# Kernel optimization log

Measured on AMD Instinct MI355X. Metric: run time of the kernel, lower is better.

The kernel has to match this reference:

```python
import jax, jax.numpy as jnp
import numpy as np

E, NB, B, N = 2, 2, 8, 512          # experts, blocks per stack, batch, nodes
SEQ_LEN, CIN, CONV, END = 12, 2, 32, 64
NFE1, SS1 = 4, 0.25                  # outer (backward-time) Euler steps / step size
NFE2, SS2 = 2, 0.5                   # graph-diffusion Euler steps / step size
RF = max(SEQ_LEN, NFE1 * 6 + CIN)    # receptive field = 26 (max kernel 7 -> shrink 6/step)


def setup_inputs() -> dict:
    ks = iter(jax.random.split(jax.random.key(0), 64))

    def nrm(shape, s=0.1):
        return jax.random.normal(next(ks), shape, dtype=jnp.float32) * s

    inp = {
        "X": jax.random.normal(next(ks), (B, SEQ_LEN, N, CIN), dtype=jnp.float32),
        "adj": jax.random.uniform(next(ks), (N, N), dtype=jnp.float32),
        "expert_weights": jnp.ones((E,), jnp.float32),
        "W_start": nrm((E, NB, CONV, CIN)), "b_start": nrm((E, NB, CONV)),
    }
    for t in ("f", "g"):
        for k in (2, 3, 5, 7):
            inp["W_%s%d" % (t, k)] = nrm((E, NB, CONV // 4, CONV, 1, k))
        inp["b_%s" % t] = nrm((E, NB, CONV))
    for t in ("gc1", "gc2"):
        inp["W_" + t] = nrm((E, NB, CONV, (NFE2 + 1) * CONV))
        inp["b_" + t] = nrm((E, NB, CONV))
    for t in ("bc", "fc"):
        inp["W_%s1" % t] = nrm((E, NB, END, CONV)); inp["b_%s1" % t] = nrm((E, NB, END))
        inp["W_%s2" % t] = nrm((E, NB, SEQ_LEN, END)); inp["b_%s2" % t] = nrm((E, NB, SEQ_LEN))
    return inp


def _conv1x1(x, W, b):  # 1x1 Conv2d over NCHW layout
    return jnp.einsum('bchw,oc->bohw', x, W) + b[None, :, None, None]


def _inception(x, Ws, b):  # DilatedInception, dilation=1, kernels (1,2/3/5/7)
    dn = ('NCHW', 'OIHW', 'NCHW')
    ys = [jax.lax.conv_general_dilated(x, W, (1, 1), 'VALID', dimension_numbers=dn) for W in Ws]
    Lm = ys[-1].shape[3]  # crop all branches to the shortest (kernel-7) length
    return jnp.concatenate([y[..., -Lm:] for y in ys], axis=1) + b[None, :, None, None]


def _cgpode(x, A, W, b):  # Euler ODE graph diffusion, concat states, 1x1 mlp
    outs, cur = [x], x
    for _ in range(NFE2):
        cur = cur + SS2 * jnp.einsum('bcwl,vw->bcvl', cur, A)
        outs.append(cur)
    return _conv1x1(jnp.concatenate(outs, axis=1), W, b)


def _forward(X, adj, expert_weights, W_start, b_start,
             W_f2, W_f3, W_f5, W_f7, b_f, W_g2, W_g3, W_g5, W_g7, b_g,
             W_gc1, b_gc1, W_gc2, b_gc2,
             W_bc1, b_bc1, W_bc2, b_bc2, W_fc1, b_fc1, W_fc2, b_fc2):
    n = adj.shape[0]
    A1 = adj + jnp.eye(n, dtype=adj.dtype)     # set_adj: D^-1/2 (A+I) D^-1/2
    di = jnp.sum(A1, axis=1) ** -0.5
    An = di[:, None] * A1 * di[None, :]
    AnT = An.T

    def block(Xb, e, k):  # STBlock; Xb: [B, L, N, C] -> (backcast, forecast)
        x = jnp.transpose(Xb, (0, 3, 2, 1))    # [B, C, N, L]
        x = jnp.pad(x, ((0, 0), (0, 0), (0, 0), (RF - SEQ_LEN, 0)))
        x = _conv1x1(x, W_start[e, k], b_start[e, k])
        Wf = (W_f2[e, k], W_f3[e, k], W_f5[e, k], W_f7[e, k])
        Wg = (W_g2[e, k], W_g3[e, k], W_g5[e, k], W_g7[e, k])
        cur_len = RF
        for _ in range(NFE1):                  # backward-time Euler: x <- x - SS1*enc(x)
            xi = x[..., -cur_len:]             # stateful intermediate_seq_len crop
            h = jnp.tanh(_inception(xi, Wf, b_f[e, k])) * jax.nn.sigmoid(_inception(xi, Wg, b_g[e, k]))
            g = _cgpode(h, An, W_gc1[e, k], b_gc1[e, k]) + _cgpode(h, AnT, W_gc2[e, k], b_gc2[e, k])
            g = jnp.pad(g, ((0, 0), (0, 0), (0, 0), (RF - g.shape[3], 0)))
            x = x - SS1 * g
            cur_len -= 6
        x = x[..., -CIN:]                      # keep last in_dim steps
        mu = jnp.mean(x, axis=(1, 2, 3), keepdims=True)
        var = jnp.mean((x - mu) ** 2, axis=(1, 2, 3), keepdims=True)
        xn = (x - mu) * jax.lax.rsqrt(var + 1e-5)  # layer_norm over shape[1:], no affine
        bc = _conv1x1(jax.nn.relu(_conv1x1(xn, W_bc1[e, k], b_bc1[e, k])), W_bc2[e, k], b_bc2[e, k])
        fc = _conv1x1(jax.nn.relu(_conv1x1(xn, W_fc1[e, k], b_fc1[e, k])), W_fc2[e, k], b_fc2[e, k])[..., -1:]
        return bc, fc

    total = jnp.zeros((X.shape[0], SEQ_LEN, n, 1), X.dtype)
    for e in range(E):                         # independent experts (n_stacks=1 each)
        bkc = X
        fct = jnp.zeros((X.shape[0], SEQ_LEN, n, 1), X.dtype)
        for k in range(NB):                    # residual block stacking inside the stack
            b_, f_ = block(bkc, e, k)
            bkc = bkc - b_
            fct = fct + f_
        total = total + expert_weights[e] * fct
    return total


def reference(X, adj, expert_weights, W_start, b_start, W_f2, W_f3, W_f5, W_f7, b_f, W_g2, W_g3, W_g5, W_g7, b_g, W_gc1, b_gc1, W_gc2, b_gc2, W_bc1, b_bc1, W_bc2, b_bc2, W_fc1, b_fc1, W_fc2, b_fc2):
    return _forward(X, adj, expert_weights, W_start, b_start, W_f2, W_f3, W_f5, W_f7, b_f, W_g2, W_g3, W_g5, W_g7, b_g, W_gc1, b_gc1, W_gc2, b_gc2, W_bc1, b_bc1, W_bc2, b_bc2, W_fc1, b_fc1, W_fc2, b_fc2)
```

## Files before the change

### kernel.cpp

```cpp
#include <hip/hip_runtime.h>
#include <stddef.h>

#define EE 2
#define NBK 2
#define BATCH 8

typedef unsigned short ushort_t;
typedef short bf16x8 __attribute__((ext_vector_type(8)));
typedef float f32x4 __attribute__((ext_vector_type(4)));
typedef unsigned short u16x4 __attribute__((ext_vector_type(4)));

__device__ __forceinline__ ushort_t f2bf(float f) {
    unsigned int u = __float_as_uint(f);
    u += 0x7FFF + ((u >> 16) & 1);
    return (ushort_t)(u >> 16);
}
__device__ __forceinline__ float bf2f(ushort_t h) {
    return __uint_as_float(((unsigned int)h) << 16);
}

__global__ __launch_bounds__(256) void k_rowsum(const float* __restrict__ adj,
                                                float* __restrict__ di) {
    int v = blockIdx.x;
    int tid = threadIdx.x;
    float s = 0.f;
    for (int w = tid; w < 512; w += 256)
        s += adj[v * 512 + w] + (w == v ? 1.f : 0.f);
    for (int off = 32; off; off >>= 1) s += __shfl_down(s, off);
    __shared__ float red[4];
    if ((tid & 63) == 0) red[tid >> 6] = s;
    __syncthreads();
    if (tid == 0) {
        float t = red[0] + red[1] + red[2] + red[3];
        di[v] = rsqrtf(t);
    }
}

__global__ __launch_bounds__(256) void k_norm(const float* __restrict__ adj,
                                              const float* __restrict__ di,
                                              ushort_t* __restrict__ An,
                                              ushort_t* __restrict__ AnT) {
    int idx = blockIdx.x * 256 + threadIdx.x;
    int v = idx >> 9, w = idx & 511;
    float a = adj[idx] + (v == w ? 1.f : 0.f);
    ushort_t val = f2bf(di[v] * a * di[w]);
    An[idx] = val;
    AnT[w * 512 + v] = val;
}

__global__ __launch_bounds__(256) void k_An2(
    const ushort_t* __restrict__ Anb, const ushort_t* __restrict__ AnTb,
    ushort_t* __restrict__ An2, ushort_t* __restrict__ An2T) {
    int tid = threadIdx.x;
    int w = tid >> 6, lane = tid & 63;
    int l15 = lane & 15, lg = lane >> 4;
    int wbase = blockIdx.x * 256 + w * 64;
    int n0 = blockIdx.y * 64;
    f32x4 acc[4][4] = {};
    const ushort_t* Ap = Anb + (size_t)(wbase + l15) * 512 + lg * 8;
    const ushort_t* Bp = AnTb + (size_t)(n0 + l15) * 512 + lg * 8;
    bf16x8 avC[4], bvC[4], avN[4], bvN[4];
#pragma unroll
    for (int i = 0; i < 4; ++i) {
        avC[i] = *(const bf16x8*)(Ap + (size_t)i * 16 * 512);
        bvC[i] = *(const bf16x8*)(Bp + (size_t)i * 16 * 512);
    }
#pragma unroll 2
    for (int k0 = 0; k0 < 512; k0 += 32) {
        int kn = k0 + 32;
        if (kn < 512) {
#pragma unroll
            for (int i = 0; i < 4; ++i) {
                avN[i] = *(const bf16x8*)(Ap + (size_t)i * 16 * 512 + kn);
                bvN[i] = *(const bf16x8*)(Bp + (size_t)i * 16 * 512 + kn);
            }
        }
#pragma unroll
        for (int mf = 0; mf < 4; ++mf)
#pragma unroll
            for (int nf = 0; nf < 4; ++nf)
                acc[mf][nf] = __builtin_amdgcn_mfma_f32_16x16x32_bf16(
                    avC[mf], bvC[nf], acc[mf][nf], 0, 0, 0);
#pragma unroll
        for (int i = 0; i < 4; ++i) { avC[i] = avN[i]; bvC[i] = bvN[i]; }
    }
#pragma unroll
    for (int mf = 0; mf < 4; ++mf)
#pragma unroll
        for (int nf = 0; nf < 4; ++nf) {
            int col = n0 + 16 * nf + l15;
            int row0 = wbase + 16 * mf + 4 * lg;
            u16x4 q;
#pragma unroll
            for (int r = 0; r < 4; ++r) {
                ushort_t vb = f2bf(acc[mf][nf][r]);
                q[r] = vb;
                An2[(size_t)(row0 + r) * 512 + col] = vb;
            }
            *(u16x4*)(An2T + (size_t)col * 512 + row0) = q;
        }
}

__global__ __launch_bounds__(256) void k_prep(
    const float* __restrict__ Wf2, const float* __restrict__ Wf3,
    const float* __restrict__ Wf5, const float* __restrict__ Wf7,
    const float* __restrict__ Wg2, const float* __restrict__ Wg3,
    const float* __restrict__ Wg5, const float* __restrict__ Wg7,
    ushort_t* __restrict__ Wb,
    const float* __restrict__ Wgc1, const float* __restrict__ bgc1,
    const float* __restrict__ Wgc2, const float* __restrict__ bgc2,
    ushort_t* __restrict__ Amix, float* __restrict__ bsum,
    const float* __restrict__ Wb1, const float* __restrict__ Wb2,
    const float* __restrict__ Wfc1, const float* __restrict__ Wfc2,
    ushort_t* __restrict__ Whd, float* __restrict__ rS, int kb) {
    int bx = blockIdx.x;
    if (bx < 112) {
        int idx = bx * 256 + threadIdx.x;
        if (idx >= 2 * 2 * 7 * 2 * 16 * 32) return;
        int c = idx & 31;
        int t1 = idx >> 5;
        int o16 = t1 & 15;
        int t2 = t1 >> 4;
        int ot = t2 & 1;
        int t3 = t2 >> 1;
        int dt = t3 % 7;
        int t4 = t3 / 7;
        int fg = t4 & 1;
        int e = t4 >> 1;
        int ek = e * NBK + kb;
        int o = ot * 16 + o16;
        int grp = o >> 3, oo = o & 7;
        const int kstab[4] = {2, 3, 5, 7};
        int ks = kstab[grp];
        int lo = 7 - ks;
        float val = 0.f;
        if (dt >= lo) {
            int di = dt - lo;
            const float* W;
            if (grp == 0) W = (fg ? Wg2 : Wf2) + (size_t)ek * 512 + oo * 64 + c * 2 + di;
            else if (grp == 1) W = (fg ? Wg3 : Wf3) + (size_t)ek * 768 + oo * 96 + c * 3 + di;
            else if (grp == 2) W = (fg ? Wg5 : Wf5) + (size_t)ek * 1280 + oo * 160 + c * 5 + di;
            else W = (fg ? Wg7 : Wf7) + (size_t)ek * 1792 + oo * 224 + c * 7 + di;
            val = *W;
        }
        Wb[idx] = f2bf(val);
    } else if (bx < 114) {
        int e = bx - 112;
        int ek = e * NBK + kb;
        const float* W1 = Wgc1 + (size_t)ek * 32 * 96;
        const float* W2 = Wgc2 + (size_t)ek * 32 * 96;
        for (int idx = threadIdx.x; idx < 32 * 160; idx += 256) {
            int co = idx / 160, k = idx % 160;
            int slot = k >> 5, cp = k & 31;
            float val;
            if (slot == 0)
                val = W1[co * 96 + cp] + W1[co * 96 + 32 + cp] + W1[co * 96 + 64 + cp] +
                      W2[co * 96 + cp] + W2[co * 96 + 32 + cp] + W2[co * 96 + 64 + cp];
            else if (slot == 1) val = 0.5f * W1[co * 96 + 32 + cp] + W1[co * 96 + 64 + cp];
            else if (slot == 2) val = 0.25f * W1[co * 96 + 64 + cp];
            else if (slot == 3) val = 0.5f * W2[co * 96 + 32 + cp] + W2[co * 96 + 64 + cp];
            else val = 0.25f * W2[co * 96 + 64 + cp];
            Amix[((size_t)e * 32 + co) * 160 + k] = f2bf(val);
        }
        if (threadIdx.x < 32)
            bsum[e * 32 + threadIdx.x] =
                bgc1[ek * 32 + threadIdx.x] + bgc2[ek * 32 + threadIdx.x];
    } else {
        int e = bx - 114;
        int ek = e * NBK + kb;
        ushort_t* Wh = Whd + (size_t)e * 6144;
        for (int i = threadIdx.x; i < 2048; i += 256)
            Wh[i] = f2bf(Wb1[(size_t)ek * 2048 + i]);
        for (int i = threadIdx.x; i < 1024; i += 256) {
            int r = i >> 6, d = i & 63;
            Wh[2048 + i] = f2bf(r < 12 ? Wb2[(size_t)ek * 768 + r * 64 + d] : 0.f);
        }
        for (int i = threadIdx.x; i < 2048; i += 256)
            Wh[3072 + i] = f2bf(Wfc1[(size_t)ek * 2048 + i]);
        for (int i = threadIdx.x; i < 1024; i += 256) {
            int r = i >> 6, d = i & 63;
            Wh[5120 + i] = f2bf(r < 12 ? Wfc2[(size_t)ek * 768 + r * 64 + d] : 0.f);
        }
        if (threadIdx.x < 64) {
            int d = threadIdx.x;
            float s1 = 0.f, s2 = 0.f;
            for (int c = 0; c < 32; ++c) {
                s1 += Wb1[(size_t)ek * 2048 + d * 32 + c];
                s2 += Wfc1[(size_t)ek * 2048 + d * 32 + c];
            }
            rS[e * 128 + d] = s1;
            rS[e * 128 + 64 + d] = s2;
        }
    }
}

__global__ __launch_bounds__(256) void k_start(const float* __restrict__ bkc,
                                               float* __restrict__ x,
                                               ushort_t* __restrict__ xb,
                                               const float* __restrict__ Wst,
                                               const float* __restrict__ bst,
                                               int kb) {
    int n = blockIdx.x * 256 + threadIdx.x;
    int t = blockIdx.y;
    int eb = blockIdx.z;
    int e = eb >> 3;
    int ek = e * NBK + kb;
    const float* Wp = Wst + (size_t)ek * 32 * 2;
    const float* bp = bst + (size_t)ek * 32;
    float in0 = 0.f, in1 = 0.f;
    if (t >= 14) {
        const float* p = bkc + ((size_t)(eb * 12 + (t - 14)) * 512 + n) * 2;
        in0 = p[0];
        in1 = p[1];
    }
    float* xo = x + ((size_t)(eb * 26 + t) * 32) * 512 + n;
    ushort_t tmp[32];
#pragma unroll
    for (int c = 0; c < 32; ++c) {
        float v = bp[c] + Wp[c * 2] * in0 + Wp[c * 2 + 1] * in1;
        xo[(size_t)c * 512] = v;
        tmp[c] = f2bf(v);
    }
    ushort_t* xbp = xb + ((size_t)(eb * 26 + t) * 512 + n) * 32;
#pragma unroll
    for (int q = 0; q < 4; ++q)
        *(bf16x8*)(xbp + q * 8) = *(bf16x8*)(tmp + q * 8);
}

__global__ __launch_bounds__(256) void k_incept_mfma(
    const ushort_t* __restrict__ xb, ushort_t* __restrict__ h,
    ushort_t* __restrict__ buf5, const ushort_t* __restrict__ Wb,
    const float* __restrict__ bf, const float* __restrict__ bg,
    int kb, int cur_len, int L) {
    int j = blockIdx.y, eb = blockIdx.z, e = eb >> 3, ek = e * NBK + kb;
    int tid = threadIdx.x;
    int w = tid >> 6, lane = tid & 63;
    int l15 = lane & 15, lg = lane >> 4;
    int ot = w >> 1;
    int n0base = blockIdx.x * 128 + (w & 1) * 64;
    int t0 = 26 - cur_len + j;

    const ushort_t* WbE = Wb + (size_t)e * 14336;
    bf16x8 af_[7], ag_[7];
#pragma unroll
    for (int dt = 0; dt < 7; ++dt) {
        af_[dt] = *(const bf16x8*)(WbE + ((size_t)(dt * 2 + ot) * 16 + l15) * 32 + lg * 8);
        ag_[dt] = *(const bf16x8*)(WbE + 7168 + ((size_t)(dt * 2 + ot) * 16 + l15) * 32 + lg * 8);
    }
    float bfv[4], bgv[4];
#pragma unroll
    for (int r = 0; r < 4; ++r) {
        int o = ot * 16 + 4 * lg + r;
        bfv[r] = bf[ek * 32 + o];
        bgv[r] = bg[ek * 32 + o];
    }
    size_t colbase = ((size_t)eb * L + j) * 32;
    size_t rowb = ((size_t)eb * L + j) * 512;
    const ushort_t* xe = xb + ((size_t)eb * 26) * 512 * 32;
#pragma unroll
    for (int nt = 0; nt < 4; ++nt) {
        int n0 = n0base + nt * 16;
        bf16x8 bfr[7];
#pragma unroll
        for (int dt = 0; dt < 7; ++dt)
            bfr[dt] = *(const bf16x8*)(xe + ((size_t)(t0 + dt) * 512 + n0 + l15) * 32 + lg * 8);
        f32x4 accf = {}, accg = {};
#pragma unroll
        for (int dt = 0; dt < 7; ++dt) {
            accf = __builtin_amdgcn_mfma_f32_16x16x32_bf16(af_[dt], bfr[dt], accf, 0, 0, 0);
            accg = __builtin_amdgcn_mfma_f32_16x16x32_bf16(ag_[dt], bfr[dt], accg, 0, 0, 0);
        }
        u16x4 q;
#pragma unroll
        for (int r = 0; r < 4; ++r) {
            float a = accf[r] + bfv[r];
            float b = accg[r] + bgv[r];
            float hv = tanhf(a) * (1.f / (1.f + expf(-b)));
            ushort_t hb = f2bf(hv);
            q[r] = hb;
            int o = ot * 16 + 4 * lg + r;
            h[(colbase + o) * 512 + n0 + l15] = hb;
        }
        *(u16x4*)(buf5 + (rowb + n0 + l15) * 160 + ot * 16 + 4 * lg) = q;
    }
}

__global__ __launch_bounds__(256) void k_gemm4(
    const ushort_t* __restrict__ A,
    const ushort_t* __restrict__ B0, const ushort_t* __restrict__ B1,
    const ushort_t* __restrict__ B2, const ushort_t* __restrict__ B3,
    ushort_t* __restrict__ buf5) {
    __shared__ __align__(16) ushort_t Bs[2][64][36];
    int z = blockIdx.z;
    const ushort_t* B = (z == 0) ? B0 : (z == 1) ? B1 : (z == 2) ? B2 : B3;
    int slot = z + 1;
    int tid = threadIdx.x;
    int w = tid >> 6, lane = tid & 63;
    int l15 = lane & 15, lg = lane >> 4;
    int wbase = blockIdx.x * 256 + w * 64;
    int n0 = blockIdx.y * 64;
    int scol = tid >> 2;
    int skq = (tid & 3) * 8;
    const ushort_t* Bsrc = B + (size_t)(n0 + scol) * 512 + skq;
    const ushort_t* Ap = A + (size_t)(wbase + l15) * 512 + lg * 8;
    f32x4 acc[4][4] = {};
    bf16x8 bregN;
    {
        bf16x8 b0r = *(const bf16x8*)(Bsrc);
        bregN = *(const bf16x8*)(Bsrc + 32);
        *(bf16x8*)&Bs[0][scol][skq] = b0r;
    }
    __syncthreads();
#pragma unroll 2
    for (int ks = 0; ks < 16; ++ks) {
        int cur = ks & 1;
        int k0 = ks * 32;
        bf16x8 av[4], bv[4];
#pragma unroll
        for (int mf = 0; mf < 4; ++mf)
            av[mf] = *(const bf16x8*)(Ap + (size_t)mf * 16 * 512 + k0);
#pragma unroll
        for (int nf = 0; nf < 4; ++nf)
            bv[nf] = *(const bf16x8*)&Bs[cur][16 * nf + l15][lg * 8];
        if (ks < 15) *(bf16x8*)&Bs[cur ^ 1][scol][skq] = bregN;
        if (ks < 14) bregN = *(const bf16x8*)(Bsrc + (ks + 2) * 32);
#pragma unroll
        for (int mf = 0; mf < 4; ++mf)
#pragma unroll
            for (int nf = 0; nf < 4; ++nf)
                acc[mf][nf] = __builtin_amdgcn_mfma_f32_16x16x32_bf16(
                    av[mf], bv[nf], acc[mf][nf], 0, 0, 0);
        __syncthreads();
    }
#pragma unroll
    for (int mf = 0; mf < 4; ++mf) {
        int jeb = (wbase >> 5) + (mf >> 1);
        int c0 = 16 * (mf & 1) + 4 * lg;
#pragma unroll
        for (int nf = 0; nf < 4; ++nf) {
            int col = n0 + 16 * nf + l15;
            u16x4 q;
#pragma unroll
            for (int r = 0; r < 4; ++r) q[r] = f2bf(acc[mf][nf][r]);
            *(u16x4*)(buf5 + ((size_t)jeb * 512 + col) * 160 + slot * 32 + c0) = q;
        }
    }
}

__global__ __launch_bounds__(256) void k_combine_mfma(
    float* __restrict__ x, ushort_t* __restrict__ xb,
    const ushort_t* __restrict__ buf5, const ushort_t* __restrict__ Amix,
    const float* __restrict__ bsum, int L) {
    int j = blockIdx.x, eb = blockIdx.y, e = eb >> 3;
    int tid = threadIdx.x, wv = tid >> 6, lane = tid & 63;
    int l15 = lane & 15, lg = lane >> 4;
    int t = 26 - L + j;
    const ushort_t* Ae = Amix + (size_t)e * 32 * 160;
    bf16x8 a[2][5];
#pragma unroll
    for (int ct = 0; ct < 2; ++ct)
#pragma unroll
        for (int ks = 0; ks < 5; ++ks)
            a[ct][ks] = *(const bf16x8*)(Ae + (size_t)(ct * 16 + l15) * 160 + ks * 32 + lg * 8);
    float bs[2][4];
#pragma unroll
    for (int ct = 0; ct < 2; ++ct)
#pragma unroll
        for (int r = 0; r < 4; ++r) bs[ct][r] = bsum[e * 32 + ct * 16 + 4 * lg + r];
    size_t rowb = ((size_t)eb * L + j) * 512;
    size_t xtb = ((size_t)(eb * 26 + t) * 32) * 512;
    ushort_t* xbt = xb + ((size_t)(eb * 26 + t) * 512) * 32;
#pragma unroll
    for (int nt = 0; nt < 8; ++nt) {
        int n = wv * 128 + nt * 16 + l15;
        const ushort_t* bp = buf5 + (rowb + n) * 160 + lg * 8;
        bf16x8 b[5];
#pragma unroll
        for (int ks = 0; ks < 5; ++ks) b[ks] = *(const bf16x8*)(bp + ks * 32);
        f32x4 acc[2] = {};
#pragma unroll
        for (int ks = 0; ks < 5; ++ks) {
            acc[0] = __builtin_amdgcn_mfma_f32_16x16x32_bf16(a[0][ks], b[ks], acc[0], 0, 0, 0);
            acc[1] = __builtin_amdgcn_mfma_f32_16x16x32_bf16(a[1][ks], b[ks], acc[1], 0, 0, 0);
        }
#pragma unroll
        for (int ct = 0; ct < 2; ++ct) {
            u16x4 q;
#pragma unroll
            for (int r = 0; r < 4; ++r) {
                int co = ct * 16 + 4 * lg + r;
                float* xp = x + xtb + (size_t)co * 512 + n;
                float nv = *xp - 0.25f * (acc[ct][r] + bs[ct][r]);
                *xp = nv;
                q[r] = f2bf(nv);
            }
            *(u16x4*)(xbt + (size_t)n * 32 + ct * 16 + 4 * lg) = q;
        }
    }
}

__global__ __launch_bounds__(256) void k_lnstats(const float* __restrict__ x,
                                                 float* __restrict__ stats) {
    int eb = blockIdx.x;
    const float* p = x + ((size_t)(eb * 26 + 24) * 32) * 512;
    float s = 0.f, s2 = 0.f;
    for (int i = threadIdx.x; i < 32768; i += 256) {
        float v = p[i];
        s += v;
        s2 += v * v;
    }
    for (int off = 32; off; off >>= 1) {
        s += __shfl_down(s, off);
        s2 += __shfl_down(s2, off);
    }
    __shared__ float r1[4], r2[4];
    if ((threadIdx.x & 63) == 0) {
        r1[threadIdx.x >> 6] = s;
        r2[threadIdx.x >> 6] = s2;
    }
    __syncthreads();
    if (threadIdx.x == 0) {
        float S = r1[0] + r1[1] + r1[2] + r1[3];
        float S2 = r2[0] + r2[1] + r2[2] + r2[3];
        float mu = S / 32768.f;
        float var = S2 / 32768.f - mu * mu;
        stats[eb * 2] = mu;
        stats[eb * 2 + 1] = rsqrtf(var + 1e-5f);
    }
}

__global__ __launch_bounds__(256) void k_heads_mfma(
    const ushort_t* __restrict__ xb, const float* __restrict__ stats,
    float* __restrict__ bkc, float* __restrict__ acc,
    const ushort_t* __restrict__ Whd, const float* __restrict__ rS,
    const float* __restrict__ bb1, const float* __restrict__ bb2,
    const float* __restrict__ bfc1, const float* __restrict__ bfc2,
    int kb) {
    __shared__ __align__(16) ushort_t lds[4][64][72];
    int w = blockIdx.y, eb = blockIdx.z;
    int e = eb >> 3, ek = e * NBK + kb;
    int tid = threadIdx.x, wv = tid >> 6, lane = tid & 63;
    int l15 = lane & 15, lg = lane >> 4;
    int n0 = blockIdx.x * 256 + wv * 64;
    float mu = stats[eb * 2], rsv = stats[eb * 2 + 1];
    const ushort_t* Wh = Whd + (size_t)e * 6144;
    const ushort_t* xrow = xb + ((size_t)(eb * 26 + 24 + w) * 512) * 32;

#pragma unroll
    for (int head = 0; head < 2; ++head) {
        if (head == 1 && w == 0) break;
        int woff = head ? 3072 : 0;
        const float* b1 = head ? bfc1 : bb1;
        const float* b2 = head ? bfc2 : bb2;
        const float* rs1 = rS + e * 128 + (head ? 64 : 0);
        bf16x8 a1[4];
#pragma unroll
        for (int rt = 0; rt < 4; ++rt)
            a1[rt] = *(const bf16x8*)(Wh + woff + (size_t)(rt * 16 + l15) * 32 + lg * 8);
        float be[4][4];
#pragma unroll
        for (int rt = 0; rt < 4; ++rt)
#pragma unroll
            for (int r = 0; r < 4; ++r) {
                int d = rt * 16 + 4 * lg + r;
                be[rt][r] = b1[ek * 64 + d] - rsv * mu * rs1[d];
            }
#pragma unroll
        for (int nt = 0; nt < 4; ++nt) {
            bf16x8 bv = *(const bf16x8*)(xrow + (size_t)(n0 + nt * 16 + l15) * 32 + lg * 8);
            f32x4 ac[4] = {};
#pragma unroll
            for (int rt = 0; rt < 4; ++rt)
                ac[rt] = __builtin_amdgcn_mfma_f32_16x16x32_bf16(a1[rt], bv, ac[rt], 0, 0, 0);
#pragma unroll
            for (int rt = 0; rt < 4; ++rt)
#pragma unroll
                for (int r = 0; r < 4; ++r) {
                    float hv = fmaxf(rsv * ac[rt][r] + be[rt][r], 0.f);
                    lds[wv][nt * 16 + l15][rt * 16 + 4 * lg + r] = f2bf(hv);
                }
        }
        bf16x8 a2[2];
        a2[0] = *(const bf16x8*)(Wh + woff + 2048 + (size_t)l15 * 64 + lg * 8);
        a2[1] = *(const bf16x8*)(Wh + woff + 2048 + (size_t)l15 * 64 + 32 + lg * 8);
        float b2v[4];
#pragma unroll
        for (int r = 0; r < 4; ++r) {
            int s = 4 * lg + r;
            b2v[r] = (s < 12) ? b2[ek * 12 + s] : 0.f;
        }
#pragma unroll
        for (int nt = 0; nt < 4; ++nt) {
            bf16x8 b0 = *(const bf16x8*)&lds[wv][nt * 16 + l15][lg * 8];
            bf16x8 b1f = *(const bf16x8*)&lds[wv][nt * 16 + l15][32 + lg * 8];
            f32x4 ac2 = {};
            ac2 = __builtin_amdgcn_mfma_f32_16x16x32_bf16(a2[0], b0, ac2, 0, 0, 0);
            ac2 = __builtin_amdgcn_mfma_f32_16x16x32_bf16(a2[1], b1f, ac2, 0, 0, 0);
#pragma unroll
            for (int r = 0; r < 4; ++r) {
                int s = 4 * lg + r;
                if (s < 12) {
                    int n = n0 + nt * 16 + l15;
                    float val = ac2[r] + b2v[r];
                    if (head == 0)
                        bkc[((size_t)(eb * 12 + s) * 512 + n) * 2 + w] -= val;
                    else
                        acc[(size_t)(eb * 12 + s) * 512 + n] += val;
                }
            }
        }
    }
}

__global__ __launch_bounds__(256) void k_final(const float* __restrict__ acc,
                                               const float* __restrict__ ew,
                                               float* __restrict__ out) {
    int i = blockIdx.x * 256 + threadIdx.x;
    out[i] = ew[0] * acc[i] + ew[1] * acc[49152 + i];
}

extern "C" void kernel_launch(void* const* d_in, const int* in_sizes, int n_in,
                              void* d_out, int out_size, void* d_ws, size_t ws_size,
                              hipStream_t stream) {
    const float* X    = (const float*)d_in[0];
    const float* adj  = (const float*)d_in[1];
    const float* ew   = (const float*)d_in[2];
    const float* Wst  = (const float*)d_in[3];
    const float* bst  = (const float*)d_in[4];
    const float* Wf2  = (const float*)d_in[5];
    const float* Wf3  = (const float*)d_in[6];
    const float* Wf5  = (const float*)d_in[7];
    const float* Wf7  = (const float*)d_in[8];
    const float* bf   = (const float*)d_in[9];
    const float* Wg2  = (const float*)d_in[10];
    const float* Wg3  = (const float*)d_in[11];
    const float* Wg5  = (const float*)d_in[12];
    const float* Wg7  = (const float*)d_in[13];
    const float* bg   = (const float*)d_in[14];
    const float* Wgc1 = (const float*)d_in[15];
    const float* bgc1 = (const float*)d_in[16];
    const float* Wgc2 = (const float*)d_in[17];
    const float* bgc2 = (const float*)d_in[18];
    const float* Wb1  = (const float*)d_in[19];
    const float* bb1  = (const float*)d_in[20];
    const float* Wb2  = (const float*)d_in[21];
    const float* bb2  = (const float*)d_in[22];
    const float* Wfc1 = (const float*)d_in[23];
    const float* bfc1 = (const float*)d_in[24];
    const float* Wfc2 = (const float*)d_in[25];
    const float* bfc2 = (const float*)d_in[26];

    float* ws = (float*)d_ws;
    size_t off = 0;
    auto alloc = [&](size_t nf) { float* p = ws + off; off += nf; return p; };
    float* di    = alloc(512);
    ushort_t* Anb   = (ushort_t*)alloc(512 * 512 / 2);
    ushort_t* AnTb  = (ushort_t*)alloc(512 * 512 / 2);
    ushort_t* An2b  = (ushort_t*)alloc(512 * 512 / 2);
    ushort_t* An2Tb = (ushort_t*)alloc(512 * 512 / 2);
    float* bkc   = alloc((size_t)EE * BATCH * 12 * 512 * 2);
    float* acc   = alloc((size_t)EE * BATCH * 12 * 512);
    float* stats = alloc(32);
    ushort_t* Amix = (ushort_t*)alloc(2 * 32 * 160 / 2);
    float* bsum  = alloc(64);
    ushort_t* Wb = (ushort_t*)alloc(14336);
    ushort_t* Whd = (ushort_t*)alloc(6144);
    float* rSb   = alloc(256);
    float* x     = alloc((size_t)16 * 26 * 32 * 512);
    ushort_t* xb = (ushort_t*)alloc((size_t)16 * 26 * 512 * 32 / 2);
    size_t hbuf_f = (size_t)16 * 20 * 32 * 512 / 2;
    ushort_t* h   = (ushort_t*)alloc(hbuf_f);
    ushort_t* buf5 = (ushort_t*)alloc((size_t)16 * 20 * 512 * 160 / 2);
    if (off * sizeof(float) > ws_size) return;

    k_rowsum<<<512, 256, 0, stream>>>(adj, di);
    k_norm<<<1024, 256, 0, stream>>>(adj, di, Anb, AnTb);
    k_An2<<<dim3(2, 8), 256, 0, stream>>>(Anb, AnTb, An2b, An2Tb);

    hipMemcpyAsync(bkc, X, (size_t)98304 * 4, hipMemcpyDeviceToDevice, stream);
    hipMemcpyAsync(bkc + 98304, X, (size_t)98304 * 4, hipMemcpyDeviceToDevice, stream);
    hipMemsetAsync(acc, 0, (size_t)EE * BATCH * 12 * 512 * 4, stream);

    for (int kb = 0; kb < NBK; ++kb) {
        k_prep<<<116, 256, 0, stream>>>(Wf2, Wf3, Wf5, Wf7, Wg2, Wg3, Wg5, Wg7, Wb,
                                        Wgc1, bgc1, Wgc2, bgc2, Amix, bsum,
                                        Wb1, Wb2, Wfc1, Wfc2, Whd, rSb, kb);
        k_start<<<dim3(2, 26, 16), 256, 0, stream>>>(bkc, x, xb, Wst, bst, kb);
        int cur = 26;
        for (int it = 0; it < 4; ++it) {
            int L = cur - 6;
            k_incept_mfma<<<dim3(4, L, 16), 256, 0, stream>>>(
                xb, h, buf5, Wb, bf, bg, kb, cur, L);
            k_gemm4<<<dim3(2 * L, 8, 4), 256, 0, stream>>>(
                h, Anb, An2b, AnTb, An2Tb, buf5);
            k_combine_mfma<<<dim3(L, 16), 256, 0, stream>>>(x, xb, buf5, Amix, bsum, L);
            cur -= 6;
        }
        k_lnstats<<<16, 256, 0, stream>>>(x, stats);
        k_heads_mfma<<<dim3(2, 2, 16), 256, 0, stream>>>(xb, stats, bkc, acc, Whd, rSb,
                                                         bb1, bb2, bfc1, bfc2, kb);
    }
    k_final<<<192, 256, 0, stream>>>(acc, ew, (float*)d_out);
}
```

Baseline: 759.3 us.

## Apply channel mix before graph diffusion and fuse four adjacency GEMMs into one

The 1x1 channel-mix weights (Amix) are now applied to the inception output first, inside the inception kernel. This produces a mixed-channel slice g0 plus four bf16 slices that are laid out along K. A single GEMM then multiplies those slices against a concatenated [An|An2|AnT|An2T] matrix with K=2048 and updates x and xb in its epilogue. This replaces the separate gemm4 and combine kernels, removing one launch and the wide buf5 intermediate, and shrinks the diffusion GEMM's M dimension from 160 to 32 rows per slice. In exchange it writes a larger fp32 g0 and a 2048-wide Aprime to global memory, and uses a longer K loop with a smaller grid.

```diff
diff --git a/kernel.cpp b/kernel.cpp
--- a/kernel.cpp
+++ b/kernel.cpp
@@ -38,32 +38,29 @@
 
 __global__ __launch_bounds__(256) void k_norm(const float* __restrict__ adj,
                                               const float* __restrict__ di,
-                                              ushort_t* __restrict__ An,
-                                              ushort_t* __restrict__ AnT) {
+                                              ushort_t* __restrict__ Bp) {
     int idx = blockIdx.x * 256 + threadIdx.x;
     int v = idx >> 9, w = idx & 511;
     float a = adj[idx] + (v == w ? 1.f : 0.f);
     ushort_t val = f2bf(di[v] * a * di[w]);
-    An[idx] = val;
-    AnT[w * 512 + v] = val;
-}
-
-__global__ __launch_bounds__(256) void k_An2(
-    const ushort_t* __restrict__ Anb, const ushort_t* __restrict__ AnTb,
-    ushort_t* __restrict__ An2, ushort_t* __restrict__ An2T) {
+    Bp[(size_t)v * 2048 + w] = val;
+    Bp[(size_t)w * 2048 + 1024 + v] = val;
+}
+
+__global__ __launch_bounds__(256) void k_An2(ushort_t* __restrict__ Bp) {
     int tid = threadIdx.x;
     int w = tid >> 6, lane = tid & 63;
     int l15 = lane & 15, lg = lane >> 4;
     int wbase = blockIdx.x * 256 + w * 64;
     int n0 = blockIdx.y * 64;
     f32x4 acc[4][4] = {};
-    const ushort_t* Ap = Anb + (size_t)(wbase + l15) * 512 + lg * 8;
-    const ushort_t* Bp = AnTb + (size_t)(n0 + l15) * 512 + lg * 8;
+    const ushort_t* Ap = Bp + (size_t)(wbase + l15) * 2048 + lg * 8;
+    const ushort_t* Bo = Bp + (size_t)(n0 + l15) * 2048 + 1024 + lg * 8;
     bf16x8 avC[4], bvC[4], avN[4], bvN[4];
 #pragma unroll
     for (int i = 0; i < 4; ++i) {
-        avC[i] = *(const bf16x8*)(Ap + (size_t)i * 16 * 512);
-        bvC[i] = *(const bf16x8*)(Bp + (size_t)i * 16 * 512);
+        avC[i] = *(const bf16x8*)(Ap + (size_t)i * 16 * 2048);
+        bvC[i] = *(const bf16x8*)(Bo + (size_t)i * 16 * 2048);
     }
 #pragma unroll 2
     for (int k0 = 0; k0 < 512; k0 += 32) {
@@ -71,8 +68,8 @@
         if (kn < 512) {
 #pragma unroll
             for (int i = 0; i < 4; ++i) {
-                avN[i] = *(const bf16x8*)(Ap + (size_t)i * 16 * 512 + kn);
-                bvN[i] = *(const bf16x8*)(Bp + (size_t)i * 16 * 512 + kn);
+                avN[i] = *(const bf16x8*)(Ap + (size_t)i * 16 * 2048 + kn);
+                bvN[i] = *(const bf16x8*)(Bo + (size_t)i * 16 * 2048 + kn);
             }
         }
 #pragma unroll
@@ -95,9 +92,9 @@
             for (int r = 0; r < 4; ++r) {
                 ushort_t vb = f2bf(acc[mf][nf][r]);
                 q[r] = vb;
-                An2[(size_t)(row0 + r) * 512 + col] = vb;
-            }
-            *(u16x4*)(An2T + (size_t)col * 512 + row0) = q;
+                Bp[(size_t)(row0 + r) * 2048 + 512 + col] = vb;
+            }
+            *(u16x4*)(Bp + (size_t)col * 2048 + 1536 + row0) = q;
         }
 }
 
@@ -227,17 +224,20 @@
         *(bf16x8*)(xbp + q * 8) = *(bf16x8*)(tmp + q * 8);
 }
 
-__global__ __launch_bounds__(256) void k_incept_mfma(
-    const ushort_t* __restrict__ xb, ushort_t* __restrict__ h,
-    ushort_t* __restrict__ buf5, const ushort_t* __restrict__ Wb,
+__global__ __launch_bounds__(256) void k_incept2(
+    const ushort_t* __restrict__ xb, ushort_t* __restrict__ Aprime,
+    float* __restrict__ g0, const ushort_t* __restrict__ Wb,
+    const ushort_t* __restrict__ Amix,
     const float* __restrict__ bf, const float* __restrict__ bg,
     int kb, int cur_len, int L) {
+    __shared__ __align__(16) ushort_t ht[128][36];
     int j = blockIdx.y, eb = blockIdx.z, e = eb >> 3, ek = e * NBK + kb;
     int tid = threadIdx.x;
     int w = tid >> 6, lane = tid & 63;
     int l15 = lane & 15, lg = lane >> 4;
     int ot = w >> 1;
-    int n0base = blockIdx.x * 128 + (w & 1) * 64;
+    int nloc0 = (w & 1) * 64;
+    int nbase = blockIdx.x * 128;
     int t0 = 26 - cur_len + j;
 
     const ushort_t* WbE = Wb + (size_t)e * 14336;
@@ -254,12 +254,11 @@
         bfv[r] = bf[ek * 32 + o];
         bgv[r] = bg[ek * 32 + o];
     }
-    size_t colbase = ((size_t)eb * L + j) * 32;
-    size_t rowb = ((size_t)eb * L + j) * 512;
     const ushort_t* xe = xb + ((size_t)eb * 26) * 512 * 32;
 #pragma unroll
     for (int nt = 0; nt < 4; ++nt) {
-        int n0 = n0base + nt * 16;
+        int nloc = nloc0 + nt * 16;
+        int n0 = nbase + nloc;
         bf16x8 bfr[7];
 #pragma unroll
         for (int dt = 0; dt < 7; ++dt)
@@ -275,128 +274,123 @@
         for (int r = 0; r < 4; ++r) {
             float a = accf[r] + bfv[r];
             float b = accg[r] + bgv[r];
-            float hv = tanhf(a) * (1.f / (1.f + expf(-b)));
-            ushort_t hb = f2bf(hv);
-            q[r] = hb;
-            int o = ot * 16 + 4 * lg + r;
-            h[(colbase + o) * 512 + n0 + l15] = hb;
-        }
-        *(u16x4*)(buf5 + (rowb + n0 + l15) * 160 + ot * 16 + 4 * lg) = q;
-    }
-}
-
-__global__ __launch_bounds__(256) void k_gemm4(
-    const ushort_t* __restrict__ A,
-    const ushort_t* __restrict__ B0, const ushort_t* __restrict__ B1,
-    const ushort_t* __restrict__ B2, const ushort_t* __restrict__ B3,
-    ushort_t* __restrict__ buf5) {
-    __shared__ __align__(16) ushort_t Bs[2][64][36];
-    int z = blockIdx.z;
-    const ushort_t* B = (z == 0) ? B0 : (z == 1) ? B1 : (z == 2) ? B2 : B3;
-    int slot = z + 1;
-    int tid = threadIdx.x;
-    int w = tid >> 6, lane = tid & 63;
+            q[r] = f2bf(tanhf(a) * (1.f / (1.f + expf(-b))));
+        }
+        *(u16x4*)&ht[nloc + l15][ot * 16 + 4 * lg] = q;
+    }
+    __syncthreads();
+
+    size_t ebj = (size_t)eb * L + j;
+    const f32x4 zero = {};
+    for (int s = w; s < 5; s += 4) {
+        bf16x8 am[2];
+        am[0] = *(const bf16x8*)(Amix + ((size_t)e * 32 + l15) * 160 + s * 32 + lg * 8);
+        am[1] = *(const bf16x8*)(Amix + ((size_t)e * 32 + 16 + l15) * 160 + s * 32 + lg * 8);
+#pragma unroll
+        for (int cf = 0; cf < 8; ++cf) {
+            bf16x8 bfrag = *(const bf16x8*)&ht[cf * 16 + l15][lg * 8];
+            int nglob = nbase + cf * 16 + l15;
+#pragma unroll
+            for (int mf = 0; mf < 2; ++mf) {
+                f32x4 a = __builtin_amdgcn_mfma_f32_16x16x32_bf16(am[mf], bfrag, zero, 0, 0, 0);
+#pragma unroll
+                for (int r = 0; r < 4; ++r) {
+                    int co = mf * 16 + 4 * lg + r;
+                    if (s == 0)
+                        g0[(ebj * 32 + co) * 512 + nglob] = a[r];
+                    else
+                        Aprime[ebj * 65536 + (size_t)co * 2048 + (s - 1) * 512 + nglob] =
+                            f2bf(a[r]);
+                }
+            }
+        }
+    }
+}
+
+__global__ __launch_bounds__(256) void k_gemmC(
+    float* __restrict__ x, ushort_t* __restrict__ xbuf,
+    const ushort_t* __restrict__ Aprime, const float* __restrict__ g0,
+    const ushort_t* __restrict__ Bp, const float* __restrict__ bsum, int L) {
+    __shared__ __align__(16) ushort_t Als[2][32][72];
+    int ct = blockIdx.x, j = blockIdx.y, eb = blockIdx.z, e = eb >> 3;
+    int tid = threadIdx.x, w = tid >> 6, lane = tid & 63;
     int l15 = lane & 15, lg = lane >> 4;
-    int wbase = blockIdx.x * 256 + w * 64;
-    int n0 = blockIdx.y * 64;
-    int scol = tid >> 2;
-    int skq = (tid & 3) * 8;
-    const ushort_t* Bsrc = B + (size_t)(n0 + scol) * 512 + skq;
-    const ushort_t* Ap = A + (size_t)(wbase + l15) * 512 + lg * 8;
-    f32x4 acc[4][4] = {};
-    bf16x8 bregN;
+    int t = 26 - L + j;
+    size_t ebj = (size_t)eb * L + j;
+    const ushort_t* Ab = Aprime + ebj * 65536;
+    int srow = tid >> 3;
+    int sk8 = (tid & 7) * 8;
+    const ushort_t* Asrc = Ab + (size_t)srow * 2048 + sk8;
+    int wc0 = ct * 256 + w * 64;
+
+    f32x4 acc[2][4];
+#pragma unroll
+    for (int mf = 0; mf < 2; ++mf)
+#pragma unroll
+        for (int nf = 0; nf < 4; ++nf)
+#pragma unroll
+            for (int r = 0; r < 4; ++r) {
+                int co = mf * 16 + 4 * lg + r;
+                int n = wc0 + nf * 16 + l15;
+                acc[mf][nf][r] = g0[(ebj * 32 + co) * 512 + n];
+            }
+    const ushort_t* Bcol[4];
+#pragma unroll
+    for (int nf = 0; nf < 4; ++nf)
+        Bcol[nf] = Bp + (size_t)(wc0 + nf * 16 + l15) * 2048 + lg * 8;
+
+    bf16x8 aN;
     {
-        bf16x8 b0r = *(const bf16x8*)(Bsrc);
-        bregN = *(const bf16x8*)(Bsrc + 32);
-        *(bf16x8*)&Bs[0][scol][skq] = b0r;
+        bf16x8 a0 = *(const bf16x8*)(Asrc);
+        aN = *(const bf16x8*)(Asrc + 64);
+        *(bf16x8*)&Als[0][srow][sk8] = a0;
     }
     __syncthreads();
 #pragma unroll 2
-    for (int ks = 0; ks < 16; ++ks) {
+    for (int ks = 0; ks < 32; ++ks) {
         int cur = ks & 1;
-        int k0 = ks * 32;
-        bf16x8 av[4], bv[4];
-#pragma unroll
-        for (int mf = 0; mf < 4; ++mf)
-            av[mf] = *(const bf16x8*)(Ap + (size_t)mf * 16 * 512 + k0);
+        int k0 = ks * 64;
+        bf16x8 av[2][2], bv[4][2];
+#pragma unroll
+        for (int mf = 0; mf < 2; ++mf)
+#pragma unroll
+            for (int kk = 0; kk < 2; ++kk)
+                av[mf][kk] = *(const bf16x8*)&Als[cur][mf * 16 + l15][kk * 32 + lg * 8];
 #pragma unroll
         for (int nf = 0; nf < 4; ++nf)
-            bv[nf] = *(const bf16x8*)&Bs[cur][16 * nf + l15][lg * 8];
-        if (ks < 15) *(bf16x8*)&Bs[cur ^ 1][scol][skq] = bregN;
-        if (ks < 14) bregN = *(const bf16x8*)(Bsrc + (ks + 2) * 32);
-#pragma unroll
-        for (int mf = 0; mf < 4; ++mf)
-#pragma unroll
-            for (int nf = 0; nf < 4; ++nf)
-                acc[mf][nf] = __builtin_amdgcn_mfma_f32_16x16x32_bf16(
-                    av[mf], bv[nf], acc[mf][nf], 0, 0, 0);
+#pragma unroll
+            for (int kk = 0; kk < 2; ++kk)
+                bv[nf][kk] = *(const bf16x8*)(Bcol[nf] + k0 + kk * 32);
+        if (ks < 31) *(bf16x8*)&Als[cur ^ 1][srow][sk8] = aN;
+        if (ks < 30) aN = *(const bf16x8*)(Asrc + (ks + 2) * 64);
+#pragma unroll
+        for (int kk = 0; kk < 2; ++kk)
+#pragma unroll
+            for (int mf = 0; mf < 2; ++mf)
+#pragma unroll
+                for (int nf = 0; nf < 4; ++nf)
+                    acc[mf][nf] = __builtin_amdgcn_mfma_f32_16x16x32_bf16(
+                        av[mf][kk], bv[nf][kk], acc[mf][nf], 0, 0, 0);
         __syncthreads();
     }
-#pragma unroll
-    for (int mf = 0; mf < 4; ++mf) {
-        int jeb = (wbase >> 5) + (mf >> 1);
-        int c0 = 16 * (mf & 1) + 4 * lg;
+    float* xt = x + ((size_t)(eb * 26 + t) * 32) * 512;
+    ushort_t* xbt = xbuf + ((size_t)(eb * 26 + t) * 512) * 32;
+#pragma unroll
+    for (int mf = 0; mf < 2; ++mf)
 #pragma unroll
         for (int nf = 0; nf < 4; ++nf) {
-            int col = n0 + 16 * nf + l15;
+            int n = wc0 + nf * 16 + l15;
             u16x4 q;
 #pragma unroll
-            for (int r = 0; r < 4; ++r) q[r] = f2bf(acc[mf][nf][r]);
-            *(u16x4*)(buf5 + ((size_t)jeb * 512 + col) * 160 + slot * 32 + c0) = q;
-        }
-    }
-}
-
-__global__ __launch_bounds__(256) void k_combine_mfma(
-    float* __restrict__ x, ushort_t* __restrict__ xb,
-    const ushort_t* __restrict__ buf5, const ushort_t* __restrict__ Amix,
-    const float* __restrict__ bsum, int L) {
-    int j = blockIdx.x, eb = blockIdx.y, e = eb >> 3;
-    int tid = threadIdx.x, wv = tid >> 6, lane = tid & 63;
-    int l15 = lane & 15, lg = lane >> 4;
-    int t = 26 - L + j;
-    const ushort_t* Ae = Amix + (size_t)e * 32 * 160;
-    bf16x8 a[2][5];
-#pragma unroll
-    for (int ct = 0; ct < 2; ++ct)
-#pragma unroll
-        for (int ks = 0; ks < 5; ++ks)
-            a[ct][ks] = *(const bf16x8*)(Ae + (size_t)(ct * 16 + l15) * 160 + ks * 32 + lg * 8);
-    float bs[2][4];
-#pragma unroll
-    for (int ct = 0; ct < 2; ++ct)
-#pragma unroll
-        for (int r = 0; r < 4; ++r) bs[ct][r] = bsum[e * 32 + ct * 16 + 4 * lg + r];
-    size_t rowb = ((size_t)eb * L + j) * 512;
-    size_t xtb = ((size_t)(eb * 26 + t) * 32) * 512;
-    ushort_t* xbt = xb + ((size_t)(eb * 26 + t) * 512) * 32;
-#pragma unroll
-    for (int nt = 0; nt < 8; ++nt) {
-        int n = wv * 128 + nt * 16 + l15;
-        const ushort_t* bp = buf5 + (rowb + n) * 160 + lg * 8;
-        bf16x8 b[5];
-#pragma unroll
-        for (int ks = 0; ks < 5; ++ks) b[ks] = *(const bf16x8*)(bp + ks * 32);
-        f32x4 acc[2] = {};
-#pragma unroll
-        for (int ks = 0; ks < 5; ++ks) {
-            acc[0] = __builtin_amdgcn_mfma_f32_16x16x32_bf16(a[0][ks], b[ks], acc[0], 0, 0, 0);
-            acc[1] = __builtin_amdgcn_mfma_f32_16x16x32_bf16(a[1][ks], b[ks], acc[1], 0, 0, 0);
-        }
-#pragma unroll
-        for (int ct = 0; ct < 2; ++ct) {
-            u16x4 q;
-#pragma unroll
             for (int r = 0; r < 4; ++r) {
-                int co = ct * 16 + 4 * lg + r;
-                float* xp = x + xtb + (size_t)co * 512 + n;
-                float nv = *xp - 0.25f * (acc[ct][r] + bs[ct][r]);
-                *xp = nv;
+                int co = mf * 16 + 4 * lg + r;
+                float nv = xt[(size_t)co * 512 + n] -
+                           0.25f * (acc[mf][nf][r] + bsum[e * 32 + co]);
+                xt[(size_t)co * 512 + n] = nv;
                 q[r] = f2bf(nv);
             }
-            *(u16x4*)(xbt + (size_t)n * 32 + ct * 16 + 4 * lg) = q;
-        }
-    }
+            *(u16x4*)(xbt + (size_t)n * 32 + mf * 16 + 4 * lg) = q;
+        }
 }
 
 __global__ __launch_bounds__(256) void k_lnstats(const float* __restrict__ x,
@@ -554,10 +548,7 @@
     size_t off = 0;
     auto alloc = [&](size_t nf) { float* p = ws + off; off += nf; return p; };
     float* di    = alloc(512);
-    ushort_t* Anb   = (ushort_t*)alloc(512 * 512 / 2);
-    ushort_t* AnTb  = (ushort_t*)alloc(512 * 512 / 2);
-    ushort_t* An2b  = (ushort_t*)alloc(512 * 512 / 2);
-    ushort_t* An2Tb = (ushort_t*)alloc(512 * 512 / 2);
+    ushort_t* Bp = (ushort_t*)alloc(512 * 2048 / 2);
     float* bkc   = alloc((size_t)EE * BATCH * 12 * 512 * 2);
     float* acc   = alloc((size_t)EE * BATCH * 12 * 512);
     float* stats = alloc(32);
@@ -568,14 +559,13 @@
     float* rSb   = alloc(256);
     float* x     = alloc((size_t)16 * 26 * 32 * 512);
     ushort_t* xb = (ushort_t*)alloc((size_t)16 * 26 * 512 * 32 / 2);
-    size_t hbuf_f = (size_t)16 * 20 * 32 * 512 / 2;
-    ushort_t* h   = (ushort_t*)alloc(hbuf_f);
-    ushort_t* buf5 = (ushort_t*)alloc((size_t)16 * 20 * 512 * 160 / 2);
+    ushort_t* Aprime = (ushort_t*)alloc((size_t)320 * 32 * 2048 / 2);
+    float* g0    = alloc((size_t)320 * 32 * 512);
     if (off * sizeof(float) > ws_size) return;
 
     k_rowsum<<<512, 256, 0, stream>>>(adj, di);
-    k_norm<<<1024, 256, 0, stream>>>(adj, di, Anb, AnTb);
-    k_An2<<<dim3(2, 8), 256, 0, stream>>>(Anb, AnTb, An2b, An2Tb);
+    k_norm<<<1024, 256, 0, stream>>>(adj, di, Bp);
+    k_An2<<<dim3(2, 8), 256, 0, stream>>>(Bp);
 
     hipMemcpyAsync(bkc, X, (size_t)98304 * 4, hipMemcpyDeviceToDevice, stream);
     hipMemcpyAsync(bkc + 98304, X, (size_t)98304 * 4, hipMemcpyDeviceToDevice, stream);
@@ -589,11 +579,10 @@
         int cur = 26;
         for (int it = 0; it < 4; ++it) {
             int L = cur - 6;
-            k_incept_mfma<<<dim3(4, L, 16), 256, 0, stream>>>(
-                xb, h, buf5, Wb, bf, bg, kb, cur, L);
-            k_gemm4<<<dim3(2 * L, 8, 4), 256, 0, stream>>>(
-                h, Anb, An2b, AnTb, An2Tb, buf5);
-            k_combine_mfma<<<dim3(L, 16), 256, 0, stream>>>(x, xb, buf5, Amix, bsum, L);
+            k_incept2<<<dim3(4, L, 16), 256, 0, stream>>>(
+                xb, Aprime, g0, Wb, Amix, bf, bg, kb, cur, L);
+            k_gemmC<<<dim3(2, L, 16), 256, 0, stream>>>(
+                x, xb, Aprime, g0, Bp, bsum, L);
             cur -= 6;
         }
         k_lnstats<<<16, 256, 0, stream>>>(x, stats);
```

After: 930.8 us. 22.6% more time.

## Drop fp32 residual state, fuse layernorm stats into heads, batch weight prep

Applied to the files above, without the earlier changes.

Removes the fp32 copy of the residual state x. The start and combine kernels now keep only the bf16 buffer, and combine reads the old bf16 value back to apply its update. The separate layernorm-stats kernel is removed, and each heads block recomputes the mean and variance from the bf16 data. Weight preparation for both blocks runs in one launch before the loop. This cuts global memory traffic and kernel launches, but the residual now accumulates in bf16, which loses precision, and the stats reduction is repeated in every heads block.

```diff
diff --git a/kernel.cpp b/kernel.cpp
--- a/kernel.cpp
+++ b/kernel.cpp
@@ -112,8 +112,15 @@
     ushort_t* __restrict__ Amix, float* __restrict__ bsum,
     const float* __restrict__ Wb1, const float* __restrict__ Wb2,
     const float* __restrict__ Wfc1, const float* __restrict__ Wfc2,
-    ushort_t* __restrict__ Whd, float* __restrict__ rS, int kb) {
+    ushort_t* __restrict__ Whd, float* __restrict__ rS) {
     int bx = blockIdx.x;
+    int kb = bx >= 116 ? 1 : 0;
+    bx -= kb * 116;
+    ushort_t* Wb_k = Wb + (size_t)kb * 28672;
+    ushort_t* Amix_k = Amix + (size_t)kb * 10240;
+    float* bsum_k = bsum + kb * 64;
+    ushort_t* Whd_k = Whd + (size_t)kb * 12288;
+    float* rS_k = rS + kb * 256;
     if (bx < 112) {
         int idx = bx * 256 + threadIdx.x;
         if (idx >= 2 * 2 * 7 * 2 * 16 * 32) return;
@@ -143,7 +150,7 @@
             else W = (fg ? Wg7 : Wf7) + (size_t)ek * 1792 + oo * 224 + c * 7 + di;
             val = *W;
         }
-        Wb[idx] = f2bf(val);
+        Wb_k[idx] = f2bf(val);
     } else if (bx < 114) {
         int e = bx - 112;
         int ek = e * NBK + kb;
@@ -160,15 +167,15 @@
             else if (slot == 2) val = 0.25f * W1[co * 96 + 64 + cp];
             else if (slot == 3) val = 0.5f * W2[co * 96 + 32 + cp] + W2[co * 96 + 64 + cp];
             else val = 0.25f * W2[co * 96 + 64 + cp];
-            Amix[((size_t)e * 32 + co) * 160 + k] = f2bf(val);
+            Amix_k[((size_t)e * 32 + co) * 160 + k] = f2bf(val);
         }
         if (threadIdx.x < 32)
-            bsum[e * 32 + threadIdx.x] =
+            bsum_k[e * 32 + threadIdx.x] =
                 bgc1[ek * 32 + threadIdx.x] + bgc2[ek * 32 + threadIdx.x];
     } else {
         int e = bx - 114;
         int ek = e * NBK + kb;
-        ushort_t* Wh = Whd + (size_t)e * 6144;
+        ushort_t* Wh = Whd_k + (size_t)e * 6144;
         for (int i = threadIdx.x; i < 2048; i += 256)
             Wh[i] = f2bf(Wb1[(size_t)ek * 2048 + i]);
         for (int i = threadIdx.x; i < 1024; i += 256) {
@@ -188,14 +195,13 @@
                 s1 += Wb1[(size_t)ek * 2048 + d * 32 + c];
                 s2 += Wfc1[(size_t)ek * 2048 + d * 32 + c];
             }
-            rS[e * 128 + d] = s1;
-            rS[e * 128 + 64 + d] = s2;
+            rS_k[e * 128 + d] = s1;
+            rS_k[e * 128 + 64 + d] = s2;
         }
     }
 }
 
 __global__ __launch_bounds__(256) void k_start(const float* __restrict__ bkc,
-                                               float* __restrict__ x,
                                                ushort_t* __restrict__ xb,
                                                const float* __restrict__ Wst,
                                                const float* __restrict__ bst,
@@ -213,14 +219,10 @@
         in0 = p[0];
         in1 = p[1];
     }
-    float* xo = x + ((size_t)(eb * 26 + t) * 32) * 512 + n;
     ushort_t tmp[32];
 #pragma unroll
-    for (int c = 0; c < 32; ++c) {
-        float v = bp[c] + Wp[c * 2] * in0 + Wp[c * 2 + 1] * in1;
-        xo[(size_t)c * 512] = v;
-        tmp[c] = f2bf(v);
-    }
+    for (int c = 0; c < 32; ++c)
+        tmp[c] = f2bf(bp[c] + Wp[c * 2] * in0 + Wp[c * 2 + 1] * in1);
     ushort_t* xbp = xb + ((size_t)(eb * 26 + t) * 512 + n) * 32;
 #pragma unroll
     for (int q = 0; q < 4; ++q)
@@ -348,7 +350,7 @@
 }
 
 __global__ __launch_bounds__(256) void k_combine_mfma(
-    float* __restrict__ x, ushort_t* __restrict__ xb,
+    ushort_t* __restrict__ xb,
     const ushort_t* __restrict__ buf5, const ushort_t* __restrict__ Amix,
     const float* __restrict__ bsum, int L) {
     int j = blockIdx.x, eb = blockIdx.y, e = eb >> 3;
@@ -368,7 +370,6 @@
 #pragma unroll
         for (int r = 0; r < 4; ++r) bs[ct][r] = bsum[e * 32 + ct * 16 + 4 * lg + r];
     size_t rowb = ((size_t)eb * L + j) * 512;
-    size_t xtb = ((size_t)(eb * 26 + t) * 32) * 512;
     ushort_t* xbt = xb + ((size_t)(eb * 26 + t) * 512) * 32;
 #pragma unroll
     for (int nt = 0; nt < 8; ++nt) {
@@ -385,64 +386,55 @@
         }
 #pragma unroll
         for (int ct = 0; ct < 2; ++ct) {
+            ushort_t* addr = xbt + (size_t)n * 32 + ct * 16 + 4 * lg;
+            u16x4 old = *(u16x4*)addr;
             u16x4 q;
 #pragma unroll
             for (int r = 0; r < 4; ++r) {
-                int co = ct * 16 + 4 * lg + r;
-                float* xp = x + xtb + (size_t)co * 512 + n;
-                float nv = *xp - 0.25f * (acc[ct][r] + bs[ct][r]);
-                *xp = nv;
+                float nv = bf2f(old[r]) - 0.25f * (acc[ct][r] + bs[ct][r]);
                 q[r] = f2bf(nv);
             }
-            *(u16x4*)(xbt + (size_t)n * 32 + ct * 16 + 4 * lg) = q;
-        }
-    }
-}
-
-__global__ __launch_bounds__(256) void k_lnstats(const float* __restrict__ x,
-                                                 float* __restrict__ stats) {
-    int eb = blockIdx.x;
-    const float* p = x + ((size_t)(eb * 26 + 24) * 32) * 512;
-    float s = 0.f, s2 = 0.f;
-    for (int i = threadIdx.x; i < 32768; i += 256) {
-        float v = p[i];
-        s += v;
-        s2 += v * v;
-    }
-    for (int off = 32; off; off >>= 1) {
-        s += __shfl_down(s, off);
-        s2 += __shfl_down(s2, off);
-    }
-    __shared__ float r1[4], r2[4];
-    if ((threadIdx.x & 63) == 0) {
-        r1[threadIdx.x >> 6] = s;
-        r2[threadIdx.x >> 6] = s2;
-    }
-    __syncthreads();
-    if (threadIdx.x == 0) {
-        float S = r1[0] + r1[1] + r1[2] + r1[3];
-        float S2 = r2[0] + r2[1] + r2[2] + r2[3];
-        float mu = S / 32768.f;
-        float var = S2 / 32768.f - mu * mu;
-        stats[eb * 2] = mu;
-        stats[eb * 2 + 1] = rsqrtf(var + 1e-5f);
+            *(u16x4*)addr = q;
+        }
     }
 }
 
 __global__ __launch_bounds__(256) void k_heads_mfma(
-    const ushort_t* __restrict__ xb, const float* __restrict__ stats,
+    const ushort_t* __restrict__ xb,
     float* __restrict__ bkc, float* __restrict__ acc,
     const ushort_t* __restrict__ Whd, const float* __restrict__ rS,
     const float* __restrict__ bb1, const float* __restrict__ bb2,
     const float* __restrict__ bfc1, const float* __restrict__ bfc2,
     int kb) {
     __shared__ __align__(16) ushort_t lds[4][64][72];
+    __shared__ float r1[4], r2[4];
     int w = blockIdx.y, eb = blockIdx.z;
     int e = eb >> 3, ek = e * NBK + kb;
     int tid = threadIdx.x, wv = tid >> 6, lane = tid & 63;
     int l15 = lane & 15, lg = lane >> 4;
     int n0 = blockIdx.x * 256 + wv * 64;
-    float mu = stats[eb * 2], rsv = stats[eb * 2 + 1];
+    const ushort_t* sp = xb + ((size_t)(eb * 26 + 24) * 512) * 32;
+    float s = 0.f, s2 = 0.f;
+    for (int i = tid * 8; i < 32768; i += 256 * 8) {
+        bf16x8 v8 = *(const bf16x8*)(sp + i);
+#pragma unroll
+        for (int q = 0; q < 8; ++q) {
+            float v = bf2f((ushort_t)v8[q]);
+            s += v;
+            s2 += v * v;
+        }
+    }
+    for (int off = 32; off; off >>= 1) {
+        s += __shfl_down(s, off);
+        s2 += __shfl_down(s2, off);
+    }
+    if ((tid & 63) == 0) { r1[tid >> 6] = s; r2[tid >> 6] = s2; }
+    __syncthreads();
+    float S = r1[0] + r1[1] + r1[2] + r1[3];
+    float S2 = r2[0] + r2[1] + r2[2] + r2[3];
+    float mu = S / 32768.f;
+    float rsv = rsqrtf(S2 / 32768.f - mu * mu + 1e-5f);
+    __syncthreads();
     const ushort_t* Wh = Whd + (size_t)e * 6144;
     const ushort_t* xrow = xb + ((size_t)(eb * 26 + 24 + w) * 512) * 32;
 
@@ -486,8 +478,8 @@
         float b2v[4];
 #pragma unroll
         for (int r = 0; r < 4; ++r) {
-            int s = 4 * lg + r;
-            b2v[r] = (s < 12) ? b2[ek * 12 + s] : 0.f;
+            int s12 = 4 * lg + r;
+            b2v[r] = (s12 < 12) ? b2[ek * 12 + s12] : 0.f;
         }
 #pragma unroll
         for (int nt = 0; nt < 4; ++nt) {
@@ -498,14 +490,14 @@
             ac2 = __builtin_amdgcn_mfma_f32_16x16x32_bf16(a2[1], b1f, ac2, 0, 0, 0);
 #pragma unroll
             for (int r = 0; r < 4; ++r) {
-                int s = 4 * lg + r;
-                if (s < 12) {
+                int s12 = 4 * lg + r;
+                if (s12 < 12) {
                     int n = n0 + nt * 16 + l15;
                     float val = ac2[r] + b2v[r];
                     if (head == 0)
-                        bkc[((size_t)(eb * 12 + s) * 512 + n) * 2 + w] -= val;
+                        bkc[((size_t)(eb * 12 + s12) * 512 + n) * 2 + w] -= val;
                     else
-                        acc[(size_t)(eb * 12 + s) * 512 + n] += val;
+                        acc[(size_t)(eb * 12 + s12) * 512 + n] += val;
                 }
             }
         }
@@ -560,13 +552,11 @@
     ushort_t* An2Tb = (ushort_t*)alloc(512 * 512 / 2);
     float* bkc   = alloc((size_t)EE * BATCH * 12 * 512 * 2);
     float* acc   = alloc((size_t)EE * BATCH * 12 * 512);
-    float* stats = alloc(32);
-    ushort_t* Amix = (ushort_t*)alloc(2 * 32 * 160 / 2);
-    float* bsum  = alloc(64);
-    ushort_t* Wb = (ushort_t*)alloc(14336);
-    ushort_t* Whd = (ushort_t*)alloc(6144);
-    float* rSb   = alloc(256);
-    float* x     = alloc((size_t)16 * 26 * 32 * 512);
+    ushort_t* Amix = (ushort_t*)alloc(2 * 10240 / 2);
+    float* bsum  = alloc(128);
+    ushort_t* Wb = (ushort_t*)alloc(2 * 28672 / 2);
+    ushort_t* Whd = (ushort_t*)alloc(2 * 12288 / 2);
+    float* rSb   = alloc(512);
     ushort_t* xb = (ushort_t*)alloc((size_t)16 * 26 * 512 * 32 / 2);
     size_t hbuf_f = (size_t)16 * 20 * 32 * 512 / 2;
     ushort_t* h   = (ushort_t*)alloc(hbuf_f);
@@ -576,29 +566,30 @@
     k_rowsum<<<512, 256, 0, stream>>>(adj, di);
     k_norm<<<1024, 256, 0, stream>>>(adj, di, Anb, AnTb);
     k_An2<<<dim3(2, 8), 256, 0, stream>>>(Anb, AnTb, An2b, An2Tb);
+    k_prep<<<232, 256, 0, stream>>>(Wf2, Wf3, Wf5, Wf7, Wg2, Wg3, Wg5, Wg7, Wb,
+                                    Wgc1, bgc1, Wgc2, bgc2, Amix, bsum,
+                                    Wb1, Wb2, Wfc1, Wfc2, Whd, rSb);
 
     hipMemcpyAsync(bkc, X, (size_t)98304 * 4, hipMemcpyDeviceToDevice, stream);
     hipMemcpyAsync(bkc + 98304, X, (size_t)98304 * 4, hipMemcpyDeviceToDevice, stream);
     hipMemsetAsync(acc, 0, (size_t)EE * BATCH * 12 * 512 * 4, stream);
 
     for (int kb = 0; kb < NBK; ++kb) {
-        k_prep<<<116, 256, 0, stream>>>(Wf2, Wf3, Wf5, Wf7, Wg2, Wg3, Wg5, Wg7, Wb,
-                                        Wgc1, bgc1, Wgc2, bgc2, Amix, bsum,
-                                        Wb1, Wb2, Wfc1, Wfc2, Whd, rSb, kb);
-        k_start<<<dim3(2, 26, 16), 256, 0, stream>>>(bkc, x, xb, Wst, bst, kb);
+        k_start<<<dim3(2, 26, 16), 256, 0, stream>>>(bkc, xb, Wst, bst, kb);
         int cur = 26;
         for (int it = 0; it < 4; ++it) {
             int L = cur - 6;
             k_incept_mfma<<<dim3(4, L, 16), 256, 0, stream>>>(
-                xb, h, buf5, Wb, bf, bg, kb, cur, L);
+                xb, h, buf5, Wb + (size_t)kb * 28672, bf, bg, kb, cur, L);
             k_gemm4<<<dim3(2 * L, 8, 4), 256, 0, stream>>>(
                 h, Anb, An2b, AnTb, An2Tb, buf5);
-            k_combine_mfma<<<dim3(L, 16), 256, 0, stream>>>(x, xb, buf5, Amix, bsum, L);
+            k_combine_mfma<<<dim3(L, 16), 256, 0, stream>>>(
+                xb, buf5, Amix + (size_t)kb * 10240, bsum + kb * 64, L);
             cur -= 6;
         }
-        k_lnstats<<<16, 256, 0, stream>>>(x, stats);
-        k_heads_mfma<<<dim3(2, 2, 16), 256, 0, stream>>>(xb, stats, bkc, acc, Whd, rSb,
-                                                         bb1, bb2, bfc1, bfc2, kb);
+        k_heads_mfma<<<dim3(2, 2, 16), 256, 0, stream>>>(
+            xb, bkc, acc, Whd + (size_t)kb * 12288, rSb + kb * 256,
+            bb1, bb2, bfc1, bfc2, kb);
     }
     k_final<<<192, 256, 0, stream>>>(acc, ew, (float*)d_out);
 }
```

New measurement: 632.2 us. 1.2x faster.
